# Performance work log

Measured on AMD Instinct MI355X. Metric: run time of the kernel, lower is better.

The kernel has to match this reference:

```python
import jax, jax.numpy as jnp
import numpy as np

NUM_OPS = 100_000
NUM_MACH = 512
H = 128
OPF = 6
MF = 2
L = 2
N_PREC = 800_000
N_CHALF = 800_000  # compat edges per direction
EPS = 1e-5


def setup_inputs() -> dict:
    key = jax.random.key(0)
    ks = jax.random.split(key, 20)
    op_features = jax.random.normal(ks[0], (NUM_OPS, OPF), dtype=jnp.float32)
    machine_features = jax.random.normal(ks[1], (NUM_MACH, MF), dtype=jnp.float32)
    prec_src = jax.random.randint(ks[2], (N_PREC,), 0, NUM_OPS, dtype=jnp.int32)
    prec_tgt = jax.random.randint(ks[3], (N_PREC,), 0, NUM_OPS, dtype=jnp.int32)
    precedence_edges = jnp.stack([prec_src, prec_tgt])  # [2, N_PREC]
    op_idx = jax.random.randint(ks[4], (N_CHALF,), 0, NUM_OPS, dtype=jnp.int32)
    m_idx = jax.random.randint(ks[5], (N_CHALF,), 0, NUM_MACH, dtype=jnp.int32)
    # bidirectional pairs in unified node space (machines offset by NUM_OPS)
    src = jnp.concatenate([op_idx, m_idx + NUM_OPS])
    tgt = jnp.concatenate([m_idx + NUM_OPS, op_idx])
    compatibility_edges = jnp.stack([src, tgt])  # [2, 2*N_CHALF]
    s = 0.05
    op_emb_W = jax.random.normal(ks[6], (H, OPF), dtype=jnp.float32) * s
    op_emb_b = jnp.zeros((H,), jnp.float32)
    mach_emb_W = jax.random.normal(ks[7], (H, MF), dtype=jnp.float32) * s
    mach_emb_b = jnp.zeros((H,), jnp.float32)
    prec_W = jax.random.normal(ks[8], (L, H, H), dtype=jnp.float32) * s
    prec_b = jax.random.normal(ks[9], (L, H), dtype=jnp.float32) * s
    compat_W = jax.random.normal(ks[10], (L, H, H), dtype=jnp.float32) * s
    compat_b = jax.random.normal(ks[11], (L, H), dtype=jnp.float32) * s
    op_ln_g = jnp.ones((L, H), jnp.float32)
    op_ln_b = jnp.zeros((L, H), jnp.float32)
    mach_ln_g = jnp.ones((L, H), jnp.float32)
    mach_ln_b = jnp.zeros((L, H), jnp.float32)
    return dict(op_features=op_features, machine_features=machine_features,
                precedence_edges=precedence_edges, compatibility_edges=compatibility_edges,
                op_emb_W=op_emb_W, op_emb_b=op_emb_b, mach_emb_W=mach_emb_W, mach_emb_b=mach_emb_b,
                prec_W=prec_W, prec_b=prec_b, compat_W=compat_W, compat_b=compat_b,
                op_ln_g=op_ln_g, op_ln_b=op_ln_b, mach_ln_g=mach_ln_g, mach_ln_b=mach_ln_b)


def _layer_norm(x, g, b):
    mu = jnp.mean(x, axis=-1, keepdims=True)
    var = jnp.mean(jnp.square(x - mu), axis=-1, keepdims=True)
    return (x - mu) * jax.lax.rsqrt(var + EPS) * g + b


def _scatter_mean(vals, idx, mask, n):
    # vals [E,H], idx [E], mask [E] bool (or None); mean over incoming edges, count clamped >= 1
    if mask is not None:
        vals = jnp.where(mask[:, None], vals, 0.0)
        idx = jnp.where(mask, idx, 0)
        ones = mask.astype(vals.dtype)
    else:
        ones = jnp.ones(idx.shape, vals.dtype)
    sums = jax.ops.segment_sum(vals, idx, num_segments=n)
    cnts = jax.ops.segment_sum(ones, idx, num_segments=n)
    return sums / jnp.maximum(cnts, 1.0)[:, None]


def _forward(op_features, machine_features, precedence_edges, compatibility_edges,
             op_emb_W, op_emb_b, mach_emb_W, mach_emb_b,
             prec_W, prec_b, compat_W, compat_b,
             op_ln_g, op_ln_b, mach_ln_g, mach_ln_b):
    num_ops = op_features.shape[0]
    num_mach = machine_features.shape[0]
    op_emb = op_features @ op_emb_W.T + op_emb_b
    mach_emb = machine_features @ mach_emb_W.T + mach_emb_b

    p_src, p_tgt = precedence_edges[0], precedence_edges[1]
    c_src, c_tgt = compatibility_edges[0], compatibility_edges[1]
    op2m = (c_src < num_ops) & (c_tgt >= num_ops)
    m2o = (c_src >= num_ops) & (c_tgt < num_ops)
    o2m_src = jnp.where(op2m, c_src, 0)
    o2m_tgt = jnp.where(op2m, c_tgt - num_ops, 0)
    m2o_src = jnp.where(m2o, c_src - num_ops, 0)
    m2o_tgt = jnp.where(m2o, c_tgt, 0)

    for l in range(L):
        # precedence (op -> op): linear-then-gather == gather-then-linear
        op_t = op_emb @ prec_W[l].T + prec_b[l]            # [num_ops, H]
        op_emb_prec = _scatter_mean(op_t[p_src], p_tgt, None, num_ops)
        # compatibility, shared linear for both directions
        op_c = op_emb @ compat_W[l].T + compat_b[l]        # [num_ops, H]
        mach_c = mach_emb @ compat_W[l].T + compat_b[l]    # [num_mach, H]
        mach_emb_compat = _scatter_mean(op_c[o2m_src], o2m_tgt, op2m, num_mach)
        op_emb_compat = _scatter_mean(mach_c[m2o_src], m2o_tgt, m2o, num_ops)
        op_emb = _layer_norm(op_emb + op_emb_prec + op_emb_compat, op_ln_g[l], op_ln_b[l])
        mach_emb = _layer_norm(mach_emb + mach_emb_compat, mach_ln_g[l], mach_ln_b[l])
    return op_emb, mach_emb


def reference(op_features, machine_features, precedence_edges, compatibility_edges,
              op_emb_W, op_emb_b, mach_emb_W, mach_emb_b,
              prec_W, prec_b, compat_W, compat_b,
              op_ln_g, op_ln_b, mach_ln_g, mach_ln_b):
    return _forward(op_features, machine_features, precedence_edges, compatibility_edges,
                    op_emb_W, op_emb_b, mach_emb_W, mach_emb_b,
                    prec_W, prec_b, compat_W, compat_b,
                    op_ln_g, op_ln_b, mach_ln_g, mach_ln_b)
```

## Files before the change

### kernel.cpp

```cpp
#include <hip/hip_runtime.h>
#include <hip/hip_bf16.h>

#define NUM_OPS   100000
#define NUM_MACH  512
#define HDIM      128
#define P1        100352
#define NHIST     200704
#define NBLK      196
#define NCOARSE   784
#define NBC       256
#define NBM       256
#define MHWORDS   (NUM_MACH * NBM)
#define NBLK_M    128
#define NBLK_T    (NBLK + NBLK_M)
#define NB_PREP   1024

typedef short short8 __attribute__((ext_vector_type(8)));
typedef unsigned short ushort8 __attribute__((ext_vector_type(8)));
typedef float floatx4 __attribute__((ext_vector_type(4)));

__device__ __forceinline__ unsigned short f2bf(float f) {
    unsigned u = __float_as_uint(f);
    unsigned r = (u + 0x7FFFu + ((u >> 16) & 1u)) >> 16;
    return (unsigned short)r;
}
__device__ __forceinline__ float bf2f(unsigned short u) {
    return __uint_as_float(((unsigned)u) << 16);
}

__global__ __launch_bounds__(256) void k_front(const int* __restrict__ prec_e, int nprec,
                                               const int* __restrict__ comp_e, int E, int M,
                                               int* __restrict__ chist_bh,
                                               int* __restrict__ mach_bh,
                                               const float* __restrict__ Fo, const float* __restrict__ Fm,
                                               const float* __restrict__ Wo, const float* __restrict__ bo,
                                               const float* __restrict__ Wm, const float* __restrict__ bm,
                                               const float* __restrict__ Wp, const float* __restrict__ Wc,
                                               unsigned short* __restrict__ op_ebf,
                                               float* __restrict__ mach_emb,
                                               unsigned short* __restrict__ mach_ebf,
                                               unsigned short* __restrict__ Wb,
                                               float* __restrict__ mach_sum) {
    int t = threadIdx.x;
    if (blockIdx.x >= NBC) {
        const int T0 = NUM_OPS * HDIM;
        const int T1 = T0 + NUM_MACH * HDIM;
        const int T2 = T1 + 2 * 128 * 256;
        const int T3 = T2 + NUM_MACH * HDIM;
        int stride = NB_PREP * 256;
        for (int idx = (blockIdx.x - NBC) * 256 + t; idx < T3; idx += stride) {
            if (idx < T0) {
                int r = idx >> 7, h = idx & 127;
                const float* f = Fo + (size_t)r * 6;
                const float* w = Wo + (size_t)h * 6;
                float s = bo[h];
#pragma unroll
                for (int i = 0; i < 6; ++i) s += f[i] * w[i];
                op_ebf[idx] = f2bf(s);
            } else if (idx < T1) {
                int j = idx - T0;
                int r = j >> 7, h = j & 127;
                const float* f = Fm + (size_t)r * 2;
                const float* w = Wm + (size_t)h * 2;
                float s = bm[h] + f[0] * w[0] + f[1] * w[1];
                mach_emb[j] = s;
                mach_ebf[j] = f2bf(s);
            } else if (idx < T2) {
                int j = idx - T1;
                int l = j >> 15, h = (j >> 8) & 127, k = j & 255;
                float v = (k < 128) ? Wp[(size_t)l * 16384 + h * 128 + k]
                                    : Wc[(size_t)l * 16384 + h * 128 + (k - 128)];
                Wb[j] = f2bf(v);
            } else {
                mach_sum[idx - T2] = 0.f;
            }
        }
        return;
    }

    __shared__ int hc[NCOARSE];
    __shared__ int hm[NUM_MACH];
    for (int i = t; i < NCOARSE; i += 256) hc[i] = 0;
    for (int i = t; i < NUM_MACH; i += 256) hm[i] = 0;
    __syncthreads();
    int NT = nprec + E;
    int ch = (NT + NBC - 1) / NBC;
    int i0 = blockIdx.x * ch, i1 = min(NT, i0 + ch);
    for (int i = i0 + t; i < i1; i += 256) {
        int key;
        if (i < nprec) key = prec_e[nprec + i];
        else {
            int e = i - nprec;
            key = P1 + comp_e[e];
            atomicAdd(&hm[comp_e[E + e] - M], 1);
        }
        atomicAdd(&hc[key >> 8], 1);
    }
    __syncthreads();
    for (int i = t; i < NCOARSE; i += 256)
        chist_bh[i * NBC + blockIdx.x] = hc[i];
    for (int i = t; i < NUM_MACH; i += 256)
        mach_bh[i * NBC + blockIdx.x] = hm[i];
}

__global__ __launch_bounds__(256) void k_cfill(const int* __restrict__ prec_e, int nprec,
                                               const int* __restrict__ comp_e, int E, int M,
                                               const int* __restrict__ scan,
                                               int* __restrict__ pairs) {
    __shared__ int cur[NCOARSE];
    for (int i = threadIdx.x; i < NCOARSE; i += 256) cur[i] = scan[i * NBC + blockIdx.x];
    __syncthreads();
    int NT = nprec + E;
    int ch = (NT + NBC - 1) / NBC;
    int i0 = blockIdx.x * ch, i1 = min(NT, i0 + ch);
    for (int i = i0 + threadIdx.x; i < i1; i += 256) {
        int key, val;
        if (i < nprec) { key = prec_e[nprec + i]; val = prec_e[i]; }
        else { int e = i - nprec; key = P1 + comp_e[e]; val = comp_e[E + e] - M; }
        int pos = atomicAdd(&cur[key >> 8], 1);
        pairs[pos] = (val << 8) | (key & 255);
    }
}

__global__ __launch_bounds__(256) void k_blocksum(const int* __restrict__ arr, int* __restrict__ partial) {
    __shared__ int sh[256];
    int b = blockIdx.x, t = threadIdx.x;
    int4 v = *(const int4*)(arr + b * 1024 + t * 4);
    sh[t] = v.x + v.y + v.z + v.w;
    __syncthreads();
    for (int o = 128; o; o >>= 1) { if (t < o) sh[t] += sh[t + o]; __syncthreads(); }
    if (!t) partial[b] = sh[0];
}

__global__ __launch_bounds__(256) void k_scanpart(const int* __restrict__ partial,
                                                  int* __restrict__ block_off) {
    __shared__ int sh[256];
    int t = threadIdx.x;
    int seg0 = blockIdx.x ? NBLK : 0;
    int n    = blockIdx.x ? NBLK_M : NBLK;
    int v = (t < n) ? partial[seg0 + t] : 0;
    sh[t] = v; __syncthreads();
    for (int o = 1; o < 256; o <<= 1) {
        int x = (t >= o) ? sh[t - o] : 0; __syncthreads();
        sh[t] += x; __syncthreads();
    }
    if (t < n) block_off[seg0 + t] = sh[t] - v;
}

__global__ __launch_bounds__(256) void k_scanwrite(const int* __restrict__ arr,
                                                   const int* __restrict__ block_off,
                                                   int* __restrict__ rs) {
    __shared__ int sh[256];
    int b = blockIdx.x, t = threadIdx.x;
    int base_i = b * 1024 + t * 4;
    int4 v = *(const int4*)(arr + base_i);
    int tsum = v.x + v.y + v.z + v.w;
    sh[t] = tsum; __syncthreads();
    for (int o = 1; o < 256; o <<= 1) {
        int x = (t >= o) ? sh[t - o] : 0; __syncthreads();
        sh[t] += x; __syncthreads();
    }
    int off = block_off[b] + sh[t] - tsum;
    int4 r; r.x = off; r.y = off + v.x; r.z = off + v.x + v.y; r.w = off + v.x + v.y + v.z;
    *(int4*)(rs + base_i) = r;
}

__global__ __launch_bounds__(256) void k_finefill(const int* __restrict__ scans, int NT,
                                                  const int* __restrict__ pairs,
                                                  int* __restrict__ rs,
                                                  int* __restrict__ bucket_all,
                                                  const int* __restrict__ comp_e, int E, int M,
                                                  int* __restrict__ bucket_mach,
                                                  int* __restrict__ mach_rs) {
    int t = threadIdx.x;
    if (blockIdx.x < NCOARSE) {
        __shared__ int hh[256];
        __shared__ int ex[256];
        __shared__ int cu[256];
        int b = blockIdx.x;
        int s = scans[b * NBC];
        int e = (b == NCOARSE - 1) ? NT : scans[(b + 1) * NBC];
        hh[t] = 0;
        __syncthreads();
        for (int i = s + t; i < e; i += 256) atomicAdd(&hh[pairs[i] & 255], 1);
        __syncthreads();
        int v = hh[t];
        ex[t] = v; __syncthreads();
        for (int o = 1; o < 256; o <<= 1) {
            int x = (t >= o) ? ex[t - o] : 0; __syncthreads();
            ex[t] += x; __syncthreads();
        }
        int start = s + ex[t] - v;
        rs[b * 256 + t] = start;
        cu[t] = start;
        __syncthreads();
        for (int i = s + t; i < e; i += 256) {
            int p = pairs[i];
            int pos = atomicAdd(&cu[p & 255], 1);
            bucket_all[pos] = ((unsigned)p) >> 8;
        }
    } else {
        __shared__ int cur[NUM_MACH];
        int blk = blockIdx.x - NCOARSE;
        const int* moff = scans + NHIST;
        for (int i = t; i < NUM_MACH; i += 256) cur[i] = moff[i * NBM + blk];
        if (blk == 0) {
            for (int m = t; m < NUM_MACH; m += 256) mach_rs[m] = moff[m * NBM];
            if (t == 0) mach_rs[NUM_MACH] = E;
        }
        __syncthreads();
        int nprec = NT - E;
        int chNT = (NT + NBC - 1) / NBC;
        int e0 = blk * chNT - nprec;       if (e0 < 0) e0 = 0;
        int e1 = (blk + 1) * chNT - nprec; if (e1 > E) e1 = E;
        for (int e = e0 + t; e < e1; e += 256) {
            int m = comp_e[E + e] - M;
            int op = comp_e[e];
            int pos = atomicAdd(&cur[m], 1);
            bucket_mach[pos] = op;
        }
    }
}

#define ACC8(acc, v) { _Pragma("unroll") for (int k = 0; k < 8; ++k) acc[k] += bf2f((unsigned short)v[k]); }

__global__ __launch_bounds__(256) void k_aggmg(
    const unsigned short* __restrict__ op_ebf, const unsigned short* __restrict__ mach_ebf,
    const int* __restrict__ rs, const int* __restrict__ bucket_all,
    unsigned short* __restrict__ Ab, int* __restrict__ flags, int M,
    const int* __restrict__ mach_rs, const int* __restrict__ bucket_mach,
    float* __restrict__ mach_sum, int nb_agg) {
    int wave = threadIdx.x >> 6, lane = threadIdx.x & 63;
    int g = lane >> 4;
    int d = (lane & 15) * 8;

    if ((int)blockIdx.x < nb_agg) {
        int r = blockIdx.x * 4 + wave;
        if (r >= M) return;
        int sA = rs[r],      eA = rs[r + 1];
        int sB = rs[P1 + r], eB = rs[P1 + r + 1];

        float a[8], b[8];
#pragma unroll
        for (int k = 0; k < 8; ++k) { a[k] = 0.f; b[k] = 0.f; }

        int baseA = sA, baseB = sB;
        while (baseA < eA || baseB < eB) {
            int cA = (baseA < eA) ? min(64, eA - baseA) : 0;
            int cB = (baseB < eB) ? min(64, eB - baseB) : 0;
            int idxA = (lane < cA) ? bucket_all[baseA + lane] : 0;
            int idxB = (lane < cB) ? bucket_all[baseB + lane] : 0;
            int jm = max(cA, cB);
            for (int j = 0; j < jm; j += 8) {
                int j0 = j + g, j1 = j + 4 + g;
                int rA0 = __shfl(idxA, j0);
                int rA1 = __shfl(idxA, j1);
                int rB0 = __shfl(idxB, j0);
                int rB1 = __shfl(idxB, j1);
                short8 vA0 = *(const short8*)(op_ebf   + (size_t)rA0 * HDIM + d);
                short8 vA1 = *(const short8*)(op_ebf   + (size_t)rA1 * HDIM + d);
                short8 vB0 = *(const short8*)(mach_ebf + (size_t)rB0 * HDIM + d);
                short8 vB1 = *(const short8*)(mach_ebf + (size_t)rB1 * HDIM + d);
                if (j0 < cA) ACC8(a, vA0);
                if (j1 < cA) ACC8(a, vA1);
                if (j0 < cB) ACC8(b, vB0);
                if (j1 < cB) ACC8(b, vB1);
            }
            baseA += 64; baseB += 64;
        }
#pragma unroll
        for (int k = 0; k < 8; ++k) {
            a[k] += __shfl_xor(a[k], 16);
            a[k] += __shfl_xor(a[k], 32);
            b[k] += __shfl_xor(b[k], 16);
            b[k] += __shfl_xor(b[k], 32);
        }
        float pinv = 1.f / fmaxf((float)(eA - sA), 1.f);
        float cinv = 1.f / fmaxf((float)(eB - sB), 1.f);

        if (lane < 16) {
            ushort8 pa, pb;
#pragma unroll
            for (int k = 0; k < 8; ++k) { pa[k] = f2bf(a[k] * pinv); pb[k] = f2bf(b[k] * cinv); }
            *(ushort8*)(Ab + (size_t)r * 256 + d)       = pa;
            *(ushort8*)(Ab + (size_t)r * 256 + 128 + d) = pb;
        }
        if (lane == 0) flags[r] = (eA > sA ? 1 : 0) | (eB > sB ? 2 : 0);
        return;
    }

    int b2 = blockIdx.x - nb_agg;
    int m  = b2 & 511;
    int yq = b2 >> 9;
    int s0 = mach_rs[m], e0 = mach_rs[m + 1];
    float a[8];
#pragma unroll
    for (int k = 0; k < 8; ++k) a[k] = 0.f;

    for (int base = s0 + (yq * 4 + wave) * 64; base < e0; base += 1024) {
        int cnt = min(64, e0 - base);
        int idx = (lane < cnt) ? bucket_mach[base + lane] : 0;
        int j = 0;
        for (; j + 16 <= cnt; j += 16) {
            int r0 = __shfl(idx, j + g);
            int r1 = __shfl(idx, j + 4 + g);
            int r2 = __shfl(idx, j + 8 + g);
            int r3 = __shfl(idx, j + 12 + g);
            short8 v0 = *(const short8*)(op_ebf + (size_t)r0 * HDIM + d);
            short8 v1 = *(const short8*)(op_ebf + (size_t)r1 * HDIM + d);
            short8 v2 = *(const short8*)(op_ebf + (size_t)r2 * HDIM + d);
            short8 v3 = *(const short8*)(op_ebf + (size_t)r3 * HDIM + d);
            ACC8(a, v0); ACC8(a, v1); ACC8(a, v2); ACC8(a, v3);
        }
        for (; j < cnt; j += 4) {
            int jj = j + g;
            int rowi = __shfl(idx, jj);
            short8 v = *(const short8*)(op_ebf + (size_t)rowi * HDIM + d);
            if (jj < cnt) ACC8(a, v);
        }
    }
#pragma unroll
    for (int k = 0; k < 8; ++k) {
        a[k] += __shfl_xor(a[k], 16);
        a[k] += __shfl_xor(a[k], 32);
    }
    if (lane < 16) {
#pragma unroll
        for (int k = 0; k < 8; ++k)
            atomicAdd(&mach_sum[m * HDIM + d + k], a[k]);
    }
}

__global__ __launch_bounds__(256) void k_gemm_mupd(
    const unsigned short* __restrict__ Ab, const unsigned short* __restrict__ embb,
    const unsigned short* __restrict__ Wb,
    const float* __restrict__ bp, const float* __restrict__ bc,
    const int* __restrict__ flags,
    const float* __restrict__ g, const float* __restrict__ bt,
    float* __restrict__ dstf, unsigned short* __restrict__ dstb, int M, int nb_gemm,
    const float* __restrict__ mach_emb, float* __restrict__ mach_sum,
    const int* __restrict__ mach_rs,
    const float* __restrict__ Wc,
    const float* __restrict__ gm, const float* __restrict__ btm,
    float* __restrict__ mdst, unsigned short* __restrict__ mdstb) {
    if ((int)blockIdx.x >= nb_gemm) {
        __shared__ float row[HDIM];
        __shared__ float red[4];
        int m = blockIdx.x - nb_gemm, t = threadIdx.x;
        int cnt = mach_rs[m + 1] - mach_rs[m];
        float sc = (cnt > 0) ? 1.f / (float)cnt : 0.f;
        if (t < HDIM) {
            row[t] = mach_sum[m * HDIM + t] * sc;
            mach_sum[m * HDIM + t] = 0.f;
        }
        __syncthreads();
        float x = 0.f, s = 0.f, q = 0.f;
        if (t < HDIM) {
            float dot = bc[t];
            const float* w = Wc + (size_t)t * HDIM;
#pragma unroll 8
            for (int k = 0; k < HDIM; ++k) dot += row[k] * w[k];
            x = mach_emb[m * HDIM + t] + ((cnt > 0) ? dot : 0.f);
            s = x; q = x * x;
#pragma unroll
            for (int o = 32; o; o >>= 1) { s += __shfl_xor(s, o); q += __shfl_xor(q, o); }
            int wv = t >> 6;
            if ((t & 63) == 0) { red[wv * 2] = s; red[wv * 2 + 1] = q; }
        }
        __syncthreads();
        if (t < HDIM) {
            s = red[0] + red[2]; q = red[1] + red[3];
            float mu = s * (1.f / 128.f);
            float rstd = rsqrtf(fmaxf(q * (1.f / 128.f) - mu * mu, 0.f) + 1e-5f);
            float y = (x - mu) * rstd * gm[t] + btm[t];
            mdst[m * HDIM + t] = y;
            if (mdstb) mdstb[m * HDIM + t] = f2bf(y);
        }
        return;
    }

    int wave = threadIdx.x >> 6, lane = threadIdx.x & 63;
    int m0 = blockIdx.x * 64 + wave * 16;
    if (m0 >= M) return;
    int quad = lane >> 4, col = lane & 15;

    floatx4 acc[8];
#pragma unroll
    for (int t = 0; t < 8; ++t) acc[t] = (floatx4){0.f, 0.f, 0.f, 0.f};

    const short* Arow  = (const short*)(Ab + (size_t)(m0 + col) * 256);
    const short* Wbase = (const short*)Wb;

#pragma unroll
    for (int ks = 0; ks < 8; ++ks) {
        short8 a = *(const short8*)(Arow + ks * 32 + quad * 8);
#pragma unroll
        for (int t = 0; t < 8; ++t) {
            short8 b = *(const short8*)(Wbase + (size_t)(t * 16 + col) * 256 + ks * 32 + quad * 8);
            acc[t] = __builtin_amdgcn_mfma_f32_16x16x32_bf16(a, b, acc[t], 0, 0, 0);
        }
    }

    float bpv[8], bcv[8], gv[8], btv[8];
#pragma unroll
    for (int t = 0; t < 8; ++t) {
        int c = t * 16 + col;
        bpv[t] = bp[c]; bcv[t] = bc[c]; gv[t] = g[c]; btv[t] = bt[c];
    }
#pragma unroll
    for (int reg = 0; reg < 4; ++reg) {
        int r = m0 + quad * 4 + reg;
        int fl = flags[r];
        float fp = (fl & 1) ? 1.f : 0.f, fc = (fl & 2) ? 1.f : 0.f;
        float x[8]; float s = 0.f, q = 0.f;
#pragma unroll
        for (int t = 0; t < 8; ++t) {
            float v = acc[t][reg] + bf2f(embb[(size_t)r * HDIM + t * 16 + col]) + fp * bpv[t] + fc * bcv[t];
            x[t] = v; s += v; q += v * v;
        }
#pragma unroll
        for (int msk = 1; msk < 16; msk <<= 1) { s += __shfl_xor(s, msk); q += __shfl_xor(q, msk); }
        float mu = s * (1.f / 128.f);
        float rstd = rsqrtf(fmaxf(q * (1.f / 128.f) - mu * mu, 0.f) + 1e-5f);
#pragma unroll
        for (int t = 0; t < 8; ++t) {
            float y = (x[t] - mu) * rstd * gv[t] + btv[t];
            if (dstf) dstf[(size_t)r * HDIM + t * 16 + col] = y;
            if (dstb) dstb[(size_t)r * HDIM + t * 16 + col] = f2bf(y);
        }
    }
}

extern "C" void kernel_launch(void* const* d_in, const int* in_sizes, int n_in,
                              void* d_out, int out_size, void* d_ws, size_t ws_size,
                              hipStream_t stream) {
    const float* op_feat    = (const float*)d_in[0];
    const float* m_feat     = (const float*)d_in[1];
    const int*   prec_e     = (const int*)d_in[2];
    const int*   comp_e     = (const int*)d_in[3];
    const float* op_emb_W   = (const float*)d_in[4];
    const float* op_emb_b   = (const float*)d_in[5];
    const float* mach_emb_W = (const float*)d_in[6];
    const float* mach_emb_b = (const float*)d_in[7];
    const float* prec_W     = (const float*)d_in[8];
    const float* prec_b     = (const float*)d_in[9];
    const float* compat_W   = (const float*)d_in[10];
    const float* compat_b   = (const float*)d_in[11];
    const float* op_ln_g    = (const float*)d_in[12];
    const float* op_ln_b    = (const float*)d_in[13];
    const float* mach_ln_g  = (const float*)d_in[14];
    const float* mach_ln_b  = (const float*)d_in[15];
    float* out = (float*)d_out;

    const int M = NUM_OPS, NM = NUM_MACH;
    const int nprec = in_sizes[2] / 2;
    const int ncomp = in_sizes[3] / 2;
    const int E = ncomp / 2;
    const int NT = nprec + E;

    float* ws = (float*)d_ws;
    size_t o = 0;
    unsigned short* op_ebf = (unsigned short*)(ws + o); o += (size_t)M * 64;
    unsigned short* Ab = (unsigned short*)(ws + o); o += (size_t)M * 128;
    unsigned short* Wb = (unsigned short*)(ws + o); o += 32768;
    float* mach_emb = ws + o; o += (size_t)NM * HDIM;
    unsigned short* mach_ebf = (unsigned short*)(ws + o); o += (size_t)NM * 64;
    float* mach_sum = ws + o; o += (size_t)NM * HDIM;
    int* ip = (int*)(ws + o);
    size_t io = 0;
    int* hists     = ip + io; io += NHIST + MHWORDS;
    int* scans     = ip + io; io += NHIST + MHWORDS;
    int* rs        = ip + io; io += NHIST;
    int* mach_rs   = ip + io; io += NM + 8;
    int* partialT  = ip + io; io += 512;
    int* block_off = ip + io; io += 512;
    int* flags     = ip + io; io += M;
    int* pairs     = ip + io; io += (size_t)NT;
    int* bucket_all  = ip + io; io += (size_t)NT;
    int* bucket_mach = ip + io; io += (size_t)E;

    int* mach_bh = hists + NHIST;

    k_front<<<NBC + NB_PREP, 256, 0, stream>>>(prec_e, nprec, comp_e, E, M, hists, mach_bh,
                                               op_feat, m_feat, op_emb_W, op_emb_b,
                                               mach_emb_W, mach_emb_b, prec_W, compat_W,
                                               op_ebf, mach_emb, mach_ebf, Wb, mach_sum);
    k_blocksum<<<NBLK_T, 256, 0, stream>>>(hists, partialT);
    k_scanpart<<<2, 256, 0, stream>>>(partialT, block_off);
    k_scanwrite<<<NBLK_T, 256, 0, stream>>>(hists, block_off, scans);
    k_cfill<<<NBC, 256, 0, stream>>>(prec_e, nprec, comp_e, E, M, scans, pairs);
    k_finefill<<<NCOARSE + NBM, 256, 0, stream>>>(scans, NT, pairs, rs, bucket_all,
                                                  comp_e, E, M, bucket_mach, mach_rs);

    const int nb_agg = (M + 3) / 4;
    const int nb_gemm = (M + 63) / 64;
    for (int l = 0; l < 2; ++l) {
        int last = (l == 1);
        const float* bpl = prec_b   + (size_t)l * HDIM;
        const float* Wc  = compat_W + (size_t)l * HDIM * HDIM;
        const float* bcl = compat_b + (size_t)l * HDIM;

        k_aggmg<<<nb_agg + NM * 4, 256, 0, stream>>>(
            op_ebf, mach_ebf, rs, bucket_all, Ab, flags, M,
            mach_rs, bucket_mach, mach_sum, nb_agg);

        k_gemm_mupd<<<nb_gemm + NM, 256, 0, stream>>>(
            Ab, op_ebf, Wb + (size_t)l * 128 * 256, bpl, bcl, flags,
            op_ln_g + (size_t)l * HDIM, op_ln_b + (size_t)l * HDIM,
            last ? out : nullptr, last ? nullptr : op_ebf, M, nb_gemm,
            mach_emb, mach_sum, mach_rs, Wc,
            mach_ln_g + (size_t)l * HDIM, mach_ln_b + (size_t)l * HDIM,
            last ? (out + (size_t)M * HDIM) : mach_emb, last ? nullptr : mach_ebf);
    }
}
```

Baseline: 513.1 us.

## Replace three-kernel scan with single-pass decoupled look-back scan

Fuses the block-sum, partial-scan and scan-write kernels into one kernel that uses a decoupled look-back: each block publishes its aggregate and inclusive prefix in a descriptor array and spins on its predecessors. The descriptor array is zeroed inside the existing front kernel. This removes two kernel launches and a round trip through the partial-sum arrays. The cost is spin-waiting, which depends on blocks being scheduled roughly in index order, and atomic polling traffic. With only 324 blocks the scan was already small, so little time is at stake.

```diff
diff --git a/kernel.cpp b/kernel.cpp
--- a/kernel.cpp
+++ b/kernel.cpp
@@ -40,15 +40,17 @@
                                                float* __restrict__ mach_emb,
                                                unsigned short* __restrict__ mach_ebf,
                                                unsigned short* __restrict__ Wb,
-                                               float* __restrict__ mach_sum) {
+                                               float* __restrict__ mach_sum,
+                                               int* __restrict__ desc_i) {
     int t = threadIdx.x;
     if (blockIdx.x >= NBC) {
         const int T0 = NUM_OPS * HDIM;
         const int T1 = T0 + NUM_MACH * HDIM;
         const int T2 = T1 + 2 * 128 * 256;
         const int T3 = T2 + NUM_MACH * HDIM;
+        const int T4 = T3 + 2 * NBLK_T;
         int stride = NB_PREP * 256;
-        for (int idx = (blockIdx.x - NBC) * 256 + t; idx < T3; idx += stride) {
+        for (int idx = (blockIdx.x - NBC) * 256 + t; idx < T4; idx += stride) {
             if (idx < T0) {
                 int r = idx >> 7, h = idx & 127;
                 const float* f = Fo + (size_t)r * 6;
@@ -71,8 +73,10 @@
                 float v = (k < 128) ? Wp[(size_t)l * 16384 + h * 128 + k]
                                     : Wc[(size_t)l * 16384 + h * 128 + (k - 128)];
                 Wb[j] = f2bf(v);
+            } else if (idx < T3) {
+                mach_sum[idx - T2] = 0.f;
             } else {
-                mach_sum[idx - T2] = 0.f;
+                desc_i[idx - T3] = 0;
             }
         }
         return;
@@ -101,6 +105,68 @@
         chist_bh[i * NBC + blockIdx.x] = hc[i];
     for (int i = t; i < NUM_MACH; i += 256)
         mach_bh[i * NBC + blockIdx.x] = hm[i];
+}
+
+#define FLAG_AGG 1ULL
+#define FLAG_INC 2ULL
+__global__ __launch_bounds__(256) void k_scan(const int* __restrict__ arr,
+                                              unsigned long long* __restrict__ desc,
+                                              int* __restrict__ scans) {
+    __shared__ int sh[256];
+    __shared__ int s_excl;
+    int b = blockIdx.x, t = threadIdx.x;
+    int base_i = b * 1024 + t * 4;
+    int4 v = *(const int4*)(arr + base_i);
+    int tsum = v.x + v.y + v.z + v.w;
+    sh[t] = tsum; __syncthreads();
+    for (int o = 1; o < 256; o <<= 1) {
+        int x = (t >= o) ? sh[t - o] : 0; __syncthreads();
+        sh[t] += x; __syncthreads();
+    }
+    int total = sh[255];
+    int seg_start = (b < NBLK) ? 0 : NBLK;
+
+    if (t == 0)
+        atomicExch(&desc[b], (FLAG_AGG << 62) | (unsigned long long)(unsigned)total);
+
+    if (t < 64) {
+        int excl = 0;
+        int i = b - 1;
+        bool done = (i < seg_start);
+        while (!done) {
+            int idx = i - t;
+            unsigned long long flag; int val;
+            if (idx >= seg_start) {
+                unsigned long long dv;
+                do { dv = atomicAdd(&desc[idx], 0ULL); flag = dv >> 62; } while (flag == 0);
+                val = (int)(unsigned)(dv & 0xFFFFFFFFULL);
+            } else { flag = FLAG_INC; val = 0; }
+            unsigned long long mask = __ballot(flag == FLAG_INC);
+            if (mask) {
+                int low = __ffsll(mask) - 1;
+                int contrib = (t <= low) ? val : 0;
+#pragma unroll
+                for (int o2 = 32; o2; o2 >>= 1) contrib += __shfl_xor(contrib, o2);
+                excl += contrib;
+                done = true;
+            } else {
+                int contrib = val;
+#pragma unroll
+                for (int o2 = 32; o2; o2 >>= 1) contrib += __shfl_xor(contrib, o2);
+                excl += contrib;
+                i -= 64;
+                done = (i < seg_start);
+            }
+        }
+        if (t == 0) {
+            s_excl = excl;
+            atomicExch(&desc[b], (FLAG_INC << 62) | (unsigned long long)(unsigned)(excl + total));
+        }
+    }
+    __syncthreads();
+    int off = s_excl + sh[t] - tsum;
+    int4 r; r.x = off; r.y = off + v.x; r.z = off + v.x + v.y; r.w = off + v.x + v.y + v.z;
+    *(int4*)(scans + base_i) = r;
 }
 
 __global__ __launch_bounds__(256) void k_cfill(const int* __restrict__ prec_e, int nprec,
@@ -120,49 +186,6 @@
         int pos = atomicAdd(&cur[key >> 8], 1);
         pairs[pos] = (val << 8) | (key & 255);
     }
-}
-
-__global__ __launch_bounds__(256) void k_blocksum(const int* __restrict__ arr, int* __restrict__ partial) {
-    __shared__ int sh[256];
-    int b = blockIdx.x, t = threadIdx.x;
-    int4 v = *(const int4*)(arr + b * 1024 + t * 4);
-    sh[t] = v.x + v.y + v.z + v.w;
-    __syncthreads();
-    for (int o = 128; o; o >>= 1) { if (t < o) sh[t] += sh[t + o]; __syncthreads(); }
-    if (!t) partial[b] = sh[0];
-}
-
-__global__ __launch_bounds__(256) void k_scanpart(const int* __restrict__ partial,
-                                                  int* __restrict__ block_off) {
-    __shared__ int sh[256];
-    int t = threadIdx.x;
-    int seg0 = blockIdx.x ? NBLK : 0;
-    int n    = blockIdx.x ? NBLK_M : NBLK;
-    int v = (t < n) ? partial[seg0 + t] : 0;
-    sh[t] = v; __syncthreads();
-    for (int o = 1; o < 256; o <<= 1) {
-        int x = (t >= o) ? sh[t - o] : 0; __syncthreads();
-        sh[t] += x; __syncthreads();
-    }
-    if (t < n) block_off[seg0 + t] = sh[t] - v;
-}
-
-__global__ __launch_bounds__(256) void k_scanwrite(const int* __restrict__ arr,
-                                                   const int* __restrict__ block_off,
-                                                   int* __restrict__ rs) {
-    __shared__ int sh[256];
-    int b = blockIdx.x, t = threadIdx.x;
-    int base_i = b * 1024 + t * 4;
-    int4 v = *(const int4*)(arr + base_i);
-    int tsum = v.x + v.y + v.z + v.w;
-    sh[t] = tsum; __syncthreads();
-    for (int o = 1; o < 256; o <<= 1) {
-        int x = (t >= o) ? sh[t - o] : 0; __syncthreads();
-        sh[t] += x; __syncthreads();
-    }
-    int off = block_off[b] + sh[t] - tsum;
-    int4 r; r.x = off; r.y = off + v.x; r.z = off + v.x + v.y; r.w = off + v.x + v.y + v.z;
-    *(int4*)(rs + base_i) = r;
 }
 
 __global__ __launch_bounds__(256) void k_finefill(const int* __restrict__ scans, int NT,
@@ -472,8 +495,7 @@
     int* scans     = ip + io; io += NHIST + MHWORDS;
     int* rs        = ip + io; io += NHIST;
     int* mach_rs   = ip + io; io += NM + 8;
-    int* partialT  = ip + io; io += 512;
-    int* block_off = ip + io; io += 512;
+    unsigned long long* desc = (unsigned long long*)(ip + io); io += 1024;
     int* flags     = ip + io; io += M;
     int* pairs     = ip + io; io += (size_t)NT;
     int* bucket_all  = ip + io; io += (size_t)NT;
@@ -484,10 +506,9 @@
     k_front<<<NBC + NB_PREP, 256, 0, stream>>>(prec_e, nprec, comp_e, E, M, hists, mach_bh,
                                                op_feat, m_feat, op_emb_W, op_emb_b,
                                                mach_emb_W, mach_emb_b, prec_W, compat_W,
-                                               op_ebf, mach_emb, mach_ebf, Wb, mach_sum);
-    k_blocksum<<<NBLK_T, 256, 0, stream>>>(hists, partialT);
-    k_scanpart<<<2, 256, 0, stream>>>(partialT, block_off);
-    k_scanwrite<<<NBLK_T, 256, 0, stream>>>(hists, block_off, scans);
+                                               op_ebf, mach_emb, mach_ebf, Wb, mach_sum,
+                                               (int*)desc);
+    k_scan<<<NBLK_T, 256, 0, stream>>>(hists, desc, scans);
     k_cfill<<<NBC, 256, 0, stream>>>(prec_e, nprec, comp_e, E, M, scans, pairs);
     k_finefill<<<NCOARSE + NBM, 256, 0, stream>>>(scans, NT, pairs, rs, bucket_all,
                                                   comp_e, E, M, bucket_mach, mach_rs);
```

New measurement: 511.3 us. Within noise of the previous version (-0.4%).
